# Kernel tuning notes

Hardware: AMD Instinct MI355X
Metric: run time of the kernel (lower is better)

The kernel has to match this reference:

```python
import jax, jax.numpy as jnp
import numpy as np

D_MODEL = 1024
N_HEADS = 16
HEAD_DIM = D_MODEL // N_HEADS


def setup_inputs() -> dict:
    key = jax.random.key(0)
    k1, k2, k3 = jax.random.split(key, 3)
    scale = 1.0 / np.sqrt(D_MODEL)
    x = jax.random.normal(k1, (4, 2048, D_MODEL), dtype=jnp.float32)
    w_qkv = jax.random.normal(k2, (D_MODEL, 3 * D_MODEL), dtype=jnp.float32) * scale
    b_qkv = jnp.zeros((3 * D_MODEL,), dtype=jnp.float32)
    w_proj = jax.random.normal(k3, (D_MODEL, D_MODEL), dtype=jnp.float32) * scale
    b_proj = jnp.zeros((D_MODEL,), dtype=jnp.float32)
    return {"x": x, "w_qkv": w_qkv, "b_qkv": b_qkv, "w_proj": w_proj, "b_proj": b_proj}


def reference(x, w_qkv, b_qkv, w_proj, b_proj):
    B, T, C = x.shape
    H, Dh = N_HEADS, HEAD_DIM
    qkv = x @ w_qkv + b_qkv                       # (B, T, 3C)
    qkv = qkv.reshape(B, T, 3, H, Dh)
    q = qkv[:, :, 0].transpose(0, 2, 1, 3)        # (B, H, T, Dh)
    k = qkv[:, :, 1].transpose(0, 2, 1, 3)
    v = qkv[:, :, 2].transpose(0, 2, 1, 3)
    att = jnp.einsum('bhqd,bhkd->bhqk', q, k) / jnp.sqrt(jnp.float32(Dh))
    causal = jnp.tril(jnp.ones((T, T), dtype=bool))
    att = jnp.where(causal[None, None], att, -jnp.inf)
    att = jax.nn.softmax(att, axis=-1)
    y = jnp.einsum('bhqk,bhkd->bhqd', att, v)     # (B, H, T, Dh)
    y = y.transpose(0, 2, 1, 3).reshape(B, T, C)
    return y @ w_proj + b_proj
```

## Files before the change

kernel.cpp:

```cpp
#include <hip/hip_runtime.h>
#include <hip/hip_bf16.h>
#include <math.h>

typedef __bf16 bf16_t;
typedef __bf16 bf16x4 __attribute__((ext_vector_type(4)));
typedef __bf16 bf16x8 __attribute__((ext_vector_type(8)));
typedef float floatx4 __attribute__((ext_vector_type(4)));
typedef unsigned int u32;

#define AS1 __attribute__((address_space(1)))
#define AS3 __attribute__((address_space(3)))

__device__ bf16_t g_xb[8192 * 1024];
__device__ bf16_t g_wqkvT[3072 * 1024];
__device__ bf16_t g_wprojT[1024 * 1024];
__device__ float  g_bqkv[3072];
__device__ float  g_bproj[1024];
__device__ bf16_t g_qkv[3ull * 64 * 2048 * 64];
#define HBREG (64ull * 2048 * 64)

__global__ __launch_bounds__(256) void cvt_x(const float* __restrict__ src,
                                             const float* __restrict__ bq,
                                             const float* __restrict__ bp) {
  int blk = blockIdx.x;
  int tid = threadIdx.x;
  if (blk < 4096) {
    int i0 = (blk * 256 + tid) * 8;
    const float4* s = (const float4*)src;
    float4 a = s[i0 / 4], b = s[i0 / 4 + 1];
    bf16x8 v;
    v[0] = (bf16_t)a.x; v[1] = (bf16_t)a.y; v[2] = (bf16_t)a.z; v[3] = (bf16_t)a.w;
    v[4] = (bf16_t)b.x; v[5] = (bf16_t)b.y; v[6] = (bf16_t)b.z; v[7] = (bf16_t)b.w;
    *(bf16x8*)&g_xb[i0] = v;
  } else if (blk == 4096) {
    for (int i = tid; i < 3072; i += 256) g_bqkv[i] = bq[i];
  } else {
    for (int i = tid; i < 1024; i += 256) g_bproj[i] = bp[i];
  }
}

__global__ __launch_bounds__(256) void tr64(const float* __restrict__ wqkv,
                                            const float* __restrict__ wproj) {
  __shared__ bf16_t tile[64][65];
  const int R = 1024;
  int bx = blockIdx.x;
  const float* in;
  bf16_t* out;
  int C, c0;
  if (bx < 48) { in = wqkv; out = g_wqkvT; C = 3072; c0 = bx * 64; }
  else         { in = wproj; out = g_wprojT; C = 1024; c0 = (bx - 48) * 64; }
  int r0 = blockIdx.y * 64;
  int tid = threadIdx.x;
#pragma unroll
  for (int it = 0; it < 16; ++it) {
    int idx = tid + it * 256;
    int r = idx >> 6, c = idx & 63;
    tile[r][c] = (bf16_t)in[(size_t)(r0 + r) * C + (c0 + c)];
  }
  __syncthreads();
#pragma unroll
  for (int it = 0; it < 16; ++it) {
    int idx = tid + it * 256;
    int r = idx >> 6, c = idx & 63;
    out[(size_t)(c0 + r) * R + (r0 + c)] = tile[c][r];
  }
}

#define MFMA16(a, b, c) __builtin_amdgcn_mfma_f32_16x16x32_bf16(a, b, c, 0, 0, 0)
#define SB0() __builtin_amdgcn_sched_barrier(0)
#define PH_MID()                                          \
  do {                                                    \
    SB0();                                                \
    __builtin_amdgcn_s_barrier();                         \
    SB0();                                                \
    asm volatile("s_waitcnt lgkmcnt(0)" ::: "memory");    \
    SB0();                                                \
  } while (0)
#define PH_END()                                          \
  do {                                                    \
    SB0();                                                \
    __builtin_amdgcn_s_barrier();                         \
    SB0();                                                \
  } while (0)

__global__ __launch_bounds__(512) void gemm256(float* __restrict__ out_ext,
                                               int M, int N, int K,
                                               int amode, int bsel, int cmode) {
  __shared__ alignas(16) bf16_t As[2][2][256 * 32];
  __shared__ alignas(16) bf16_t Bs[2][2][128 * 32];
  (void)M;
  const bf16_t* Ag = (amode == 0) ? g_xb : g_qkv;
  const bf16_t* Bt = bsel ? g_wprojT : g_wqkvT;
  const float* bias = bsel ? g_bproj : g_bqkv;
  const int tid = threadIdx.x;

  int gx = gridDim.x;
  int nwg = gx * gridDim.y;
  int lin = blockIdx.y * gx + blockIdx.x;
  int swz = (lin & 7) * (nwg >> 3) + (lin >> 3);
  int bx = swz % gx, by = swz / gx;
  const int m0 = by * 256, n0 = bx * 128;

  const int lane = tid & 63, wave = tid >> 6;
  const int wm = wave >> 1, wn = wave & 1;
  const int quad = lane >> 4, l16 = lane & 15;

  u32 L0 = (u32)tid * 16u, L1 = (u32)(tid + 512) * 16u;
  u32 y0 = L0 ^ (((L0 >> 7) & 3u) << 4);
  u32 y1 = L1 ^ (((L1 >> 7) & 3u) << 4);
  int ar0 = y0 >> 6, ac0 = (y0 & 63) >> 1;
  int ar1 = y1 >> 6, ac1 = (y1 & 63) >> 1;
  u32 a_go0, a_go1, ktstride;
  if (amode == 0) {
    a_go0 = (u32)(m0 + ar0) * (u32)K + (u32)ac0;
    a_go1 = (u32)(m0 + ar1) * (u32)K + (u32)ac1;
    ktstride = 64u;
  } else {
    int mA = m0 + ar0, bb_ = mA >> 11, tt = mA & 2047;
    a_go0 = (u32)bb_ * 2097152u + (u32)tt * 64u + (u32)ac0;
    mA = m0 + ar1; bb_ = mA >> 11; tt = mA & 2047;
    a_go1 = (u32)bb_ * 2097152u + (u32)tt * 64u + (u32)ac1;
    ktstride = 131072u;
  }
  u32 b_go = (u32)(n0 + ar0) * (u32)K + (u32)ac0;

  auto stageA = [&](int kt_, int s_) {
    int bb = kt_ & 1;
    const bf16_t* s0 = Ag + (size_t)(a_go0 + (u32)kt_ * ktstride + (u32)s_ * 32u);
    const bf16_t* s1 = Ag + (size_t)(a_go1 + (u32)kt_ * ktstride + (u32)s_ * 32u);
    __builtin_amdgcn_global_load_lds((const AS1 void*)s0,
                                     (AS3 void*)&As[bb][s_][(u32)tid * 8u], 16, 0, 0);
    __builtin_amdgcn_global_load_lds((const AS1 void*)s1,
                                     (AS3 void*)&As[bb][s_][(u32)(tid + 512) * 8u], 16, 0, 0);
  };
  auto stageB = [&](int kt_, int s_) {
    int bb = kt_ & 1;
    const bf16_t* s0 = Bt + (size_t)(b_go + (u32)kt_ * 64u + (u32)s_ * 32u);
    __builtin_amdgcn_global_load_lds((const AS1 void*)s0,
                                     (AS3 void*)&Bs[bb][s_][(u32)tid * 8u], 16, 0, 0);
  };

  int saB[4], sbB[4];
#pragma unroll
  for (int i = 0; i < 4; ++i) {
    u32 xa = (u32)(wm * 64 + i * 16 + l16) * 64u + (u32)quad * 16u;
    saB[i] = (int)(xa ^ (((xa >> 7) & 3u) << 4));
    u32 xb = (u32)(wn * 64 + i * 16 + l16) * 64u + (u32)quad * 16u;
    sbB[i] = (int)(xb ^ (((xb >> 7) & 3u) << 4));
  }

  floatx4 acc[4][4] = {};
  const int NT = K >> 6;

  stageA(0, 0); SB0(); stageB(0, 0); SB0();
  stageA(0, 1); SB0(); stageB(0, 1); SB0();
  stageA(1, 0); SB0(); stageB(1, 0); SB0();
  asm volatile("s_waitcnt vmcnt(6)" ::: "memory");
  __builtin_amdgcn_s_barrier();
  SB0();

  for (int kt = 0; kt < NT; ++kt) {
    const int b = kt & 1;
    const char* Ab0 = (const char*)&As[b][0][0];
    const char* Ab1 = (const char*)&As[b][1][0];
    const char* Bb0 = (const char*)&Bs[b][0][0];
    const char* Bb1 = (const char*)&Bs[b][1][0];
    bf16x8 a0[4], bf2[2];

#pragma unroll
    for (int i = 0; i < 4; ++i) a0[i] = *(const bf16x8*)(Ab0 + saB[i]);
    bf2[0] = *(const bf16x8*)(Bb0 + sbB[0]);
    bf2[1] = *(const bf16x8*)(Bb0 + sbB[1]);
    if (kt + 1 < NT) stageA(kt + 1, 1);
    PH_MID();
    __builtin_amdgcn_s_setprio(1);
#pragma unroll
    for (int i = 0; i < 4; ++i) {
      acc[i][0] = MFMA16(a0[i], bf2[0], acc[i][0]);
      acc[i][1] = MFMA16(a0[i], bf2[1], acc[i][1]);
    }
    __builtin_amdgcn_s_setprio(0);
    PH_END();

    bf2[0] = *(const bf16x8*)(Bb0 + sbB[2]);
    bf2[1] = *(const bf16x8*)(Bb0 + sbB[3]);
    if (kt + 1 < NT) stageB(kt + 1, 1);
    PH_MID();
    __builtin_amdgcn_s_setprio(1);
#pragma unroll
    for (int i = 0; i < 4; ++i) {
      acc[i][2] = MFMA16(a0[i], bf2[0], acc[i][2]);
      acc[i][3] = MFMA16(a0[i], bf2[1], acc[i][3]);
    }
    __builtin_amdgcn_s_setprio(0);
    SB0();
    if (kt + 1 < NT) asm volatile("s_waitcnt vmcnt(6)" ::: "memory");
    else             asm volatile("s_waitcnt vmcnt(0)" ::: "memory");
    __builtin_amdgcn_s_barrier();
    SB0();

#pragma unroll
    for (int i = 0; i < 4; ++i) a0[i] = *(const bf16x8*)(Ab1 + saB[i]);
    bf2[0] = *(const bf16x8*)(Bb1 + sbB[0]);
    bf2[1] = *(const bf16x8*)(Bb1 + sbB[1]);
    if (kt + 2 < NT) stageA(kt + 2, 0);
    PH_MID();
    __builtin_amdgcn_s_setprio(1);
#pragma unroll
    for (int i = 0; i < 4; ++i) {
      acc[i][0] = MFMA16(a0[i], bf2[0], acc[i][0]);
      acc[i][1] = MFMA16(a0[i], bf2[1], acc[i][1]);
    }
    __builtin_amdgcn_s_setprio(0);
    PH_END();

    bf2[0] = *(const bf16x8*)(Bb1 + sbB[2]);
    bf2[1] = *(const bf16x8*)(Bb1 + sbB[3]);
    if (kt + 2 < NT) stageB(kt + 2, 0);
    PH_MID();
    __builtin_amdgcn_s_setprio(1);
#pragma unroll
    for (int i = 0; i < 4; ++i) {
      acc[i][2] = MFMA16(a0[i], bf2[0], acc[i][2]);
      acc[i][3] = MFMA16(a0[i], bf2[1], acc[i][3]);
    }
    __builtin_amdgcn_s_setprio(0);
    SB0();
    if (kt + 2 < NT)      asm volatile("s_waitcnt vmcnt(6)" ::: "memory");
    else if (kt + 1 < NT) asm volatile("s_waitcnt vmcnt(3)" ::: "memory");
    else                  asm volatile("s_waitcnt vmcnt(0)" ::: "memory");
    __builtin_amdgcn_s_barrier();
    SB0();
  }

#pragma unroll
  for (int mf = 0; mf < 4; ++mf) {
#pragma unroll
    for (int nf = 0; nf < 4; ++nf) {
      int ncol = n0 + wn * 64 + nf * 16 + l16;
      float bb = bias[ncol];
      int mbase = m0 + wm * 64 + mf * 16 + quad * 4;
      if (cmode == 0) {
        int which = ncol >> 10;
        int h = (ncol >> 6) & 15;
        int d = ncol & 63;
        int b_ = mbase >> 11, t = mbase & 2047;
        if (which == 2) {
          bf16x4 pk;
#pragma unroll
          for (int r = 0; r < 4; ++r) pk[r] = (bf16_t)(acc[mf][nf][r] + bb);
          size_t dst = 2 * HBREG + ((size_t)((b_ * 16 + h) * 64 + d)) * 2048 + t;
          *(bf16x4*)&g_qkv[dst] = pk;
        } else {
          size_t base = (size_t)which * HBREG +
                        ((size_t)((b_ * 16 + h) * 2048 + t)) * 64 + d;
#pragma unroll
          for (int r = 0; r < 4; ++r)
            g_qkv[base + (size_t)r * 64] = (bf16_t)(acc[mf][nf][r] + bb);
        }
      } else {
#pragma unroll
        for (int r = 0; r < 4; ++r)
          out_ext[(size_t)(mbase + r) * N + ncol] = acc[mf][nf][r] + bb;
      }
    }
  }
}

__global__ __launch_bounds__(256) void attn64() {
  const int LDW = 72;
  __shared__ bf16_t Qs[64 * 72];
  __shared__ bf16_t Ks[64 * 72];
  __shared__ bf16_t Vt[64 * 72];
  bf16_t* Ps = Qs;
  const float C1 = 0.1803368801111204f;
  const float C2 = -23.083120654223414f;
  const int tid = threadIdx.x;
  const int qpair = blockIdx.x;
  const int bh = blockIdx.y;
  const bf16_t* Qb  = g_qkv + (size_t)bh * 2048 * 64;
  const bf16_t* Kb  = g_qkv + HBREG + (size_t)bh * 2048 * 64;
  const bf16_t* VTb = g_qkv + 2 * HBREG + (size_t)bh * 64 * 2048;
  bf16_t* Yb = g_qkv + (size_t)bh * 2048 * 64;
  const int lane = tid & 63, wave = tid >> 6;
  const int quad = lane >> 4, l16 = lane & 15;
  const int row0 = tid >> 3, c80 = (tid & 7) * 8;

  bf16x8 ones8;
#pragma unroll
  for (int j = 0; j < 8; ++j) ones8[j] = (bf16_t)1.0f;

  for (int ph = 0; ph < 2; ++ph) {
    const int qi = ph ? (31 - qpair) : qpair;
    const int q0 = qi * 64;

    *(bf16x8*)&Qs[row0 * LDW + c80] =
        *(const bf16x8*)&Qb[(size_t)(q0 + row0) * 64 + c80];
    *(bf16x8*)&Qs[(row0 + 32) * LDW + c80] =
        *(const bf16x8*)&Qb[(size_t)(q0 + row0 + 32) * 64 + c80];
    __syncthreads();
    bf16x8 aq0 = *(const bf16x8*)&Qs[(wave * 16 + l16) * LDW + quad * 8];
    bf16x8 aq1 = *(const bf16x8*)&Qs[(wave * 16 + l16) * LDW + 32 + quad * 8];

    floatx4 o[4] = {};
    floatx4 osum = {};

    bf16x8 kp0 = *(const bf16x8*)&Kb[(size_t)row0 * 64 + c80];
    bf16x8 kp1 = *(const bf16x8*)&Kb[(size_t)(row0 + 32) * 64 + c80];
    bf16x8 vp0 = *(const bf16x8*)&VTb[(size_t)row0 * 2048 + c80];
    bf16x8 vp1 = *(const bf16x8*)&VTb[(size_t)(row0 + 32) * 2048 + c80];

    const int ntiles = qi + 1;
    for (int kt = 0; kt < ntiles; ++kt) {
      __syncthreads();
      *(bf16x8*)&Ks[row0 * LDW + c80] = kp0;
      *(bf16x8*)&Ks[(row0 + 32) * LDW + c80] = kp1;
      *(bf16x8*)&Vt[row0 * LDW + c80] = vp0;
      *(bf16x8*)&Vt[(row0 + 32) * LDW + c80] = vp1;
      if (kt + 1 < ntiles) {
        const int k1 = (kt + 1) * 64;
        kp0 = *(const bf16x8*)&Kb[(size_t)(k1 + row0) * 64 + c80];
        kp1 = *(const bf16x8*)&Kb[(size_t)(k1 + row0 + 32) * 64 + c80];
        vp0 = *(const bf16x8*)&VTb[(size_t)row0 * 2048 + k1 + c80];
        vp1 = *(const bf16x8*)&VTb[(size_t)(row0 + 32) * 2048 + k1 + c80];
      }
      __syncthreads();

      const int k0 = kt * 64;
      floatx4 s[4];
#pragma unroll
      for (int tn = 0; tn < 4; ++tn) {
        bf16x8 bk0 = *(const bf16x8*)&Ks[(tn * 16 + l16) * LDW + quad * 8];
        bf16x8 bk1 = *(const bf16x8*)&Ks[(tn * 16 + l16) * LDW + 32 + quad * 8];
        floatx4 z = {};
        z = __builtin_amdgcn_mfma_f32_16x16x32_bf16(aq0, bk0, z, 0, 0, 0);
        z = __builtin_amdgcn_mfma_f32_16x16x32_bf16(aq1, bk1, z, 0, 0, 0);
        s[tn] = z;
      }

      if (kt == qi) {
#pragma unroll
        for (int tn = 0; tn < 4; ++tn) {
          int kcol = k0 + tn * 16 + l16;
#pragma unroll
          for (int r = 0; r < 4; ++r) {
            int qrow = q0 + wave * 16 + quad * 4 + r;
            float p = exp2f(fminf(fmaf(s[tn][r], C1, C2), 30.f));
            s[tn][r] = (kcol > qrow) ? 0.f : p;
          }
        }
      } else {
#pragma unroll
        for (int tn = 0; tn < 4; ++tn)
#pragma unroll
          for (int r = 0; r < 4; ++r)
            s[tn][r] = exp2f(fminf(fmaf(s[tn][r], C1, C2), 30.f));
      }

      bf16_t* Pw = &Ps[wave * 16 * LDW];
#pragma unroll
      for (int tn = 0; tn < 4; ++tn)
#pragma unroll
        for (int r = 0; r < 4; ++r)
          Pw[(quad * 4 + r) * LDW + tn * 16 + l16] = (bf16_t)s[tn][r];

      bf16x8 ap0 = *(const bf16x8*)&Pw[l16 * LDW + quad * 8];
      bf16x8 ap1 = *(const bf16x8*)&Pw[l16 * LDW + 32 + quad * 8];
#pragma unroll
      for (int tn = 0; tn < 4; ++tn) {
        bf16x8 bv0 = *(const bf16x8*)&Vt[(tn * 16 + l16) * LDW + quad * 8];
        bf16x8 bv1 = *(const bf16x8*)&Vt[(tn * 16 + l16) * LDW + 32 + quad * 8];
        o[tn] = __builtin_amdgcn_mfma_f32_16x16x32_bf16(ap0, bv0, o[tn], 0, 0, 0);
        o[tn] = __builtin_amdgcn_mfma_f32_16x16x32_bf16(ap1, bv1, o[tn], 0, 0, 0);
      }
      osum = __builtin_amdgcn_mfma_f32_16x16x32_bf16(ap0, ones8, osum, 0, 0, 0);
      osum = __builtin_amdgcn_mfma_f32_16x16x32_bf16(ap1, ones8, osum, 0, 0, 0);
    }

#pragma unroll
    for (int tn = 0; tn < 4; ++tn) {
      int d = tn * 16 + l16;
#pragma unroll
      for (int r = 0; r < 4; ++r) {
        int t = q0 + wave * 16 + quad * 4 + r;
        float v = o[tn][r] / osum[r];
        Yb[(size_t)t * 64 + d] = (bf16_t)v;
      }
    }
    __syncthreads();
  }
}

extern "C" void kernel_launch(void* const* d_in, const int* in_sizes, int n_in,
                              void* d_out, int out_size, void* d_ws, size_t ws_size,
                              hipStream_t stream) {
  const float* x      = (const float*)d_in[0];
  const float* w_qkv  = (const float*)d_in[1];
  const float* b_qkv  = (const float*)d_in[2];
  const float* w_proj = (const float*)d_in[3];
  const float* b_proj = (const float*)d_in[4];
  (void)d_ws; (void)ws_size;

  cvt_x<<<4098, 256, 0, stream>>>(x, b_qkv, b_proj);
  tr64<<<dim3(64, 16), 256, 0, stream>>>(w_qkv, w_proj);

  gemm256<<<dim3(24, 32), 512, 0, stream>>>(nullptr, 8192, 3072, 1024, 0, 0, 0);

  attn64<<<dim3(16, 64), 256, 0, stream>>>();

  gemm256<<<dim3(8, 32), 512, 0, stream>>>((float*)d_out, 8192, 1024, 1024, 1, 1, 1);
}
```

Before: 322.3 us.

## Enlarge GEMM tile to 256x256 with K64 swizzled LDS ping-pong schedule

```diff
diff --git a/kernel.cpp b/kernel.cpp
--- a/kernel.cpp
+++ b/kernel.cpp
@@ -86,8 +86,8 @@
 __global__ __launch_bounds__(512) void gemm256(float* __restrict__ out_ext,
                                                int M, int N, int K,
                                                int amode, int bsel, int cmode) {
-  __shared__ alignas(16) bf16_t As[2][2][256 * 32];
-  __shared__ alignas(16) bf16_t Bs[2][2][128 * 32];
+  __shared__ alignas(16) bf16_t As[2][256 * 64];
+  __shared__ alignas(16) bf16_t Bs[2][256 * 64];
   (void)M;
   const bf16_t* Ag = (amode == 0) ? g_xb : g_qkv;
   const bf16_t* Bt = bsel ? g_wprojT : g_wqkvT;
@@ -99,170 +99,199 @@
   int lin = blockIdx.y * gx + blockIdx.x;
   int swz = (lin & 7) * (nwg >> 3) + (lin >> 3);
   int bx = swz % gx, by = swz / gx;
-  const int m0 = by * 256, n0 = bx * 128;
+  const int m0 = by * 256, n0 = bx * 256;
 
   const int lane = tid & 63, wave = tid >> 6;
-  const int wm = wave >> 1, wn = wave & 1;
+  const int wm = wave >> 2, wn = wave & 3;
   const int quad = lane >> 4, l16 = lane & 15;
 
-  u32 L0 = (u32)tid * 16u, L1 = (u32)(tid + 512) * 16u;
-  u32 y0 = L0 ^ (((L0 >> 7) & 3u) << 4);
-  u32 y1 = L1 ^ (((L1 >> 7) & 3u) << 4);
-  int ar0 = y0 >> 6, ac0 = (y0 & 63) >> 1;
-  int ar1 = y1 >> 6, ac1 = (y1 & 63) >> 1;
-  u32 a_go0, a_go1, ktstride;
+  const u32 xv = (u32)(l16 & 7) << 4;
+  const u32 sq0 = ((u32)quad * 16u) ^ xv;
+  const u32 sq1 = (64u + (u32)quad * 16u) ^ xv;
+  const u32 a_rb = (u32)(wm * 64 + l16) * 128u;
+  const u32 b_rb = (u32)(wn * 32 + l16) * 128u;
+
+  u32 row_j[2], scol_j[2];
+#pragma unroll
+  for (int j = 0; j < 2; ++j) {
+    u32 L = ((u32)j * 512u + (u32)tid) * 16u;
+    u32 y = L ^ (((L >> 7) & 7u) << 4);
+    row_j[j] = y >> 7;
+    scol_j[j] = (y & 127u) >> 1;
+  }
+  u32 a_go[2][2], b_go[2][2], akts;
   if (amode == 0) {
-    a_go0 = (u32)(m0 + ar0) * (u32)K + (u32)ac0;
-    a_go1 = (u32)(m0 + ar1) * (u32)K + (u32)ac1;
-    ktstride = 64u;
+#pragma unroll
+    for (int h = 0; h < 2; ++h)
+#pragma unroll
+      for (int j = 0; j < 2; ++j)
+        a_go[h][j] = (u32)(m0 + h * 128 + (int)row_j[j]) * (u32)K + scol_j[j];
+    akts = 64u;
   } else {
-    int mA = m0 + ar0, bb_ = mA >> 11, tt = mA & 2047;
-    a_go0 = (u32)bb_ * 2097152u + (u32)tt * 64u + (u32)ac0;
-    mA = m0 + ar1; bb_ = mA >> 11; tt = mA & 2047;
-    a_go1 = (u32)bb_ * 2097152u + (u32)tt * 64u + (u32)ac1;
-    ktstride = 131072u;
-  }
-  u32 b_go = (u32)(n0 + ar0) * (u32)K + (u32)ac0;
-
-  auto stageA = [&](int kt_, int s_) {
-    int bb = kt_ & 1;
-    const bf16_t* s0 = Ag + (size_t)(a_go0 + (u32)kt_ * ktstride + (u32)s_ * 32u);
-    const bf16_t* s1 = Ag + (size_t)(a_go1 + (u32)kt_ * ktstride + (u32)s_ * 32u);
-    __builtin_amdgcn_global_load_lds((const AS1 void*)s0,
-                                     (AS3 void*)&As[bb][s_][(u32)tid * 8u], 16, 0, 0);
-    __builtin_amdgcn_global_load_lds((const AS1 void*)s1,
-                                     (AS3 void*)&As[bb][s_][(u32)(tid + 512) * 8u], 16, 0, 0);
+#pragma unroll
+    for (int h = 0; h < 2; ++h)
+#pragma unroll
+      for (int j = 0; j < 2; ++j) {
+        int m = m0 + h * 128 + (int)row_j[j];
+        a_go[h][j] = (u32)(m >> 11) * 2097152u + (u32)(m & 2047) * 64u + scol_j[j];
+      }
+    akts = 131072u;
+  }
+#pragma unroll
+  for (int h = 0; h < 2; ++h)
+#pragma unroll
+    for (int j = 0; j < 2; ++j)
+      b_go[h][j] = (u32)(n0 + h * 128 + (int)row_j[j]) * (u32)K + scol_j[j];
+
+  auto stageA = [&](int kt_, int h_) {
+#pragma unroll
+    for (int j = 0; j < 2; ++j)
+      __builtin_amdgcn_global_load_lds(
+          (const AS1 void*)(Ag + (size_t)(a_go[h_][j] + (u32)kt_ * akts)),
+          (AS3 void*)&As[kt_ & 1][h_ * 8192 + (j * 512 + tid) * 8], 16, 0, 0);
   };
-  auto stageB = [&](int kt_, int s_) {
-    int bb = kt_ & 1;
-    const bf16_t* s0 = Bt + (size_t)(b_go + (u32)kt_ * 64u + (u32)s_ * 32u);
-    __builtin_amdgcn_global_load_lds((const AS1 void*)s0,
-                                     (AS3 void*)&Bs[bb][s_][(u32)tid * 8u], 16, 0, 0);
+  auto stageB = [&](int kt_, int h_) {
+#pragma unroll
+    for (int j = 0; j < 2; ++j)
+      __builtin_amdgcn_global_load_lds(
+          (const AS1 void*)(Bt + (size_t)(b_go[h_][j] + (u32)kt_ * 64u)),
+          (AS3 void*)&Bs[kt_ & 1][h_ * 8192 + (j * 512 + tid) * 8], 16, 0, 0);
   };
 
-  int saB[4], sbB[4];
-#pragma unroll
-  for (int i = 0; i < 4; ++i) {
-    u32 xa = (u32)(wm * 64 + i * 16 + l16) * 64u + (u32)quad * 16u;
-    saB[i] = (int)(xa ^ (((xa >> 7) & 3u) << 4));
-    u32 xb = (u32)(wn * 64 + i * 16 + l16) * 64u + (u32)quad * 16u;
-    sbB[i] = (int)(xb ^ (((xb >> 7) & 3u) << 4));
-  }
-
-  floatx4 acc[4][4] = {};
+  floatx4 acc[2][4][2][2] = {};
   const int NT = K >> 6;
 
   stageA(0, 0); SB0(); stageB(0, 0); SB0();
   stageA(0, 1); SB0(); stageB(0, 1); SB0();
-  stageA(1, 0); SB0(); stageB(1, 0); SB0();
-  asm volatile("s_waitcnt vmcnt(6)" ::: "memory");
+  asm volatile("s_waitcnt vmcnt(4)" ::: "memory");
   __builtin_amdgcn_s_barrier();
   SB0();
 
   for (int kt = 0; kt < NT; ++kt) {
     const int b = kt & 1;
-    const char* Ab0 = (const char*)&As[b][0][0];
-    const char* Ab1 = (const char*)&As[b][1][0];
-    const char* Bb0 = (const char*)&Bs[b][0][0];
-    const char* Bb1 = (const char*)&Bs[b][1][0];
-    bf16x8 a0[4], bf2[2];
-
-#pragma unroll
-    for (int i = 0; i < 4; ++i) a0[i] = *(const bf16x8*)(Ab0 + saB[i]);
-    bf2[0] = *(const bf16x8*)(Bb0 + sbB[0]);
-    bf2[1] = *(const bf16x8*)(Bb0 + sbB[1]);
+    const char* Ab = (const char*)&As[b][0];
+    const char* Bb = (const char*)&Bs[b][0];
+    bf16x8 af[4][2], bv[2][2], bw[2][2];
+
+#pragma unroll
+    for (int mf = 0; mf < 4; ++mf) {
+      af[mf][0] = *(const bf16x8*)(Ab + (a_rb + mf * 2048 + sq0));
+      af[mf][1] = *(const bf16x8*)(Ab + (a_rb + mf * 2048 + sq1));
+    }
+#pragma unroll
+    for (int nf = 0; nf < 2; ++nf) {
+      bv[nf][0] = *(const bf16x8*)(Bb + (b_rb + nf * 2048 + sq0));
+      bv[nf][1] = *(const bf16x8*)(Bb + (b_rb + nf * 2048 + sq1));
+    }
+    if (kt + 1 < NT) stageA(kt + 1, 0);
+    PH_MID();
+    __builtin_amdgcn_s_setprio(1);
+#pragma unroll
+    for (int mf = 0; mf < 4; ++mf)
+#pragma unroll
+      for (int nf = 0; nf < 2; ++nf) {
+        acc[0][mf][0][nf] = MFMA16(af[mf][0], bv[nf][0], acc[0][mf][0][nf]);
+        acc[0][mf][0][nf] = MFMA16(af[mf][1], bv[nf][1], acc[0][mf][0][nf]);
+      }
+    __builtin_amdgcn_s_setprio(0);
+    SB0();
+    if (kt + 1 < NT) asm volatile("s_waitcnt vmcnt(2)" ::: "memory");
+    else             asm volatile("s_waitcnt vmcnt(0)" ::: "memory");
+    __builtin_amdgcn_s_barrier();
+    SB0();
+
+#pragma unroll
+    for (int nf = 0; nf < 2; ++nf) {
+      bw[nf][0] = *(const bf16x8*)(Bb + (b_rb + 16384 + nf * 2048 + sq0));
+      bw[nf][1] = *(const bf16x8*)(Bb + (b_rb + 16384 + nf * 2048 + sq1));
+    }
+    if (kt + 1 < NT) stageB(kt + 1, 0);
+    PH_MID();
+    __builtin_amdgcn_s_setprio(1);
+#pragma unroll
+    for (int mf = 0; mf < 4; ++mf)
+#pragma unroll
+      for (int nf = 0; nf < 2; ++nf) {
+        acc[0][mf][1][nf] = MFMA16(af[mf][0], bw[nf][0], acc[0][mf][1][nf]);
+        acc[0][mf][1][nf] = MFMA16(af[mf][1], bw[nf][1], acc[0][mf][1][nf]);
+      }
+    __builtin_amdgcn_s_setprio(0);
+    PH_END();
+
+#pragma unroll
+    for (int mf = 0; mf < 4; ++mf) {
+      af[mf][0] = *(const bf16x8*)(Ab + (a_rb + 16384 + mf * 2048 + sq0));
+      af[mf][1] = *(const bf16x8*)(Ab + (a_rb + 16384 + mf * 2048 + sq1));
+    }
     if (kt + 1 < NT) stageA(kt + 1, 1);
     PH_MID();
     __builtin_amdgcn_s_setprio(1);
 #pragma unroll
-    for (int i = 0; i < 4; ++i) {
-      acc[i][0] = MFMA16(a0[i], bf2[0], acc[i][0]);
-      acc[i][1] = MFMA16(a0[i], bf2[1], acc[i][1]);
-    }
+    for (int mf = 0; mf < 4; ++mf)
+#pragma unroll
+      for (int nf = 0; nf < 2; ++nf) {
+        acc[1][mf][1][nf] = MFMA16(af[mf][0], bw[nf][0], acc[1][mf][1][nf]);
+        acc[1][mf][1][nf] = MFMA16(af[mf][1], bw[nf][1], acc[1][mf][1][nf]);
+      }
     __builtin_amdgcn_s_setprio(0);
     PH_END();
 
-    bf2[0] = *(const bf16x8*)(Bb0 + sbB[2]);
-    bf2[1] = *(const bf16x8*)(Bb0 + sbB[3]);
+#pragma unroll
+    for (int nf = 0; nf < 2; ++nf) {
+      bv[nf][0] = *(const bf16x8*)(Bb + (b_rb + nf * 2048 + sq0));
+      bv[nf][1] = *(const bf16x8*)(Bb + (b_rb + nf * 2048 + sq1));
+    }
     if (kt + 1 < NT) stageB(kt + 1, 1);
     PH_MID();
     __builtin_amdgcn_s_setprio(1);
 #pragma unroll
-    for (int i = 0; i < 4; ++i) {
-      acc[i][2] = MFMA16(a0[i], bf2[0], acc[i][2]);
-      acc[i][3] = MFMA16(a0[i], bf2[1], acc[i][3]);
-    }
+    for (int mf = 0; mf < 4; ++mf)
+#pragma unroll
+      for (int nf = 0; nf < 2; ++nf) {
+        acc[1][mf][0][nf] = MFMA16(af[mf][0], bv[nf][0], acc[1][mf][0][nf]);
+        acc[1][mf][0][nf] = MFMA16(af[mf][1], bv[nf][1], acc[1][mf][0][nf]);
+      }
     __builtin_amdgcn_s_setprio(0);
     SB0();
-    if (kt + 1 < NT) asm volatile("s_waitcnt vmcnt(6)" ::: "memory");
+    if (kt + 1 < NT) asm volatile("s_waitcnt vmcnt(4)" ::: "memory");
     else             asm volatile("s_waitcnt vmcnt(0)" ::: "memory");
     __builtin_amdgcn_s_barrier();
     SB0();
-
-#pragma unroll
-    for (int i = 0; i < 4; ++i) a0[i] = *(const bf16x8*)(Ab1 + saB[i]);
-    bf2[0] = *(const bf16x8*)(Bb1 + sbB[0]);
-    bf2[1] = *(const bf16x8*)(Bb1 + sbB[1]);
-    if (kt + 2 < NT) stageA(kt + 2, 0);
-    PH_MID();
-    __builtin_amdgcn_s_setprio(1);
-#pragma unroll
-    for (int i = 0; i < 4; ++i) {
-      acc[i][0] = MFMA16(a0[i], bf2[0], acc[i][0]);
-      acc[i][1] = MFMA16(a0[i], bf2[1], acc[i][1]);
-    }
-    __builtin_amdgcn_s_setprio(0);
-    PH_END();
-
-    bf2[0] = *(const bf16x8*)(Bb1 + sbB[2]);
-    bf2[1] = *(const bf16x8*)(Bb1 + sbB[3]);
-    if (kt + 2 < NT) stageB(kt + 2, 0);
-    PH_MID();
-    __builtin_amdgcn_s_setprio(1);
-#pragma unroll
-    for (int i = 0; i < 4; ++i) {
-      acc[i][2] = MFMA16(a0[i], bf2[0], acc[i][2]);
-      acc[i][3] = MFMA16(a0[i], bf2[1], acc[i][3]);
-    }
-    __builtin_amdgcn_s_setprio(0);
-    SB0();
-    if (kt + 2 < NT)      asm volatile("s_waitcnt vmcnt(6)" ::: "memory");
-    else if (kt + 1 < NT) asm volatile("s_waitcnt vmcnt(3)" ::: "memory");
-    else                  asm volatile("s_waitcnt vmcnt(0)" ::: "memory");
-    __builtin_amdgcn_s_barrier();
-    SB0();
-  }
-
-#pragma unroll
-  for (int mf = 0; mf < 4; ++mf) {
-#pragma unroll
-    for (int nf = 0; nf < 4; ++nf) {
-      int ncol = n0 + wn * 64 + nf * 16 + l16;
-      float bb = bias[ncol];
-      int mbase = m0 + wm * 64 + mf * 16 + quad * 4;
-      if (cmode == 0) {
-        int which = ncol >> 10;
-        int h = (ncol >> 6) & 15;
-        int d = ncol & 63;
-        int b_ = mbase >> 11, t = mbase & 2047;
-        if (which == 2) {
-          bf16x4 pk;
-#pragma unroll
-          for (int r = 0; r < 4; ++r) pk[r] = (bf16_t)(acc[mf][nf][r] + bb);
-          size_t dst = 2 * HBREG + ((size_t)((b_ * 16 + h) * 64 + d)) * 2048 + t;
-          *(bf16x4*)&g_qkv[dst] = pk;
-        } else {
-          size_t base = (size_t)which * HBREG +
-                        ((size_t)((b_ * 16 + h) * 2048 + t)) * 64 + d;
-#pragma unroll
-          for (int r = 0; r < 4; ++r)
-            g_qkv[base + (size_t)r * 64] = (bf16_t)(acc[mf][nf][r] + bb);
-        }
+  }
+
+#pragma unroll
+  for (int mh = 0; mh < 2; ++mh)
+#pragma unroll
+  for (int mf = 0; mf < 4; ++mf)
+#pragma unroll
+  for (int nh = 0; nh < 2; ++nh)
+#pragma unroll
+  for (int nf = 0; nf < 2; ++nf) {
+    int ncol = n0 + wn * 32 + nh * 128 + nf * 16 + l16;
+    float bb = bias[ncol];
+    int mbase = m0 + wm * 64 + mh * 128 + mf * 16 + quad * 4;
+    if (cmode == 0) {
+      int which = ncol >> 10;
+      int h = (ncol >> 6) & 15;
+      int d = ncol & 63;
+      int b_ = mbase >> 11, t = mbase & 2047;
+      if (which == 2) {
+        bf16x4 pk;
+#pragma unroll
+        for (int r = 0; r < 4; ++r) pk[r] = (bf16_t)(acc[mh][mf][nh][nf][r] + bb);
+        size_t dst = 2 * HBREG + ((size_t)((b_ * 16 + h) * 64 + d)) * 2048 + t;
+        *(bf16x4*)&g_qkv[dst] = pk;
       } else {
+        size_t base = (size_t)which * HBREG +
+                      ((size_t)((b_ * 16 + h) * 2048 + t)) * 64 + d;
 #pragma unroll
         for (int r = 0; r < 4; ++r)
-          out_ext[(size_t)(mbase + r) * N + ncol] = acc[mf][nf][r] + bb;
-      }
+          g_qkv[base + (size_t)r * 64] = (bf16_t)(acc[mh][mf][nh][nf][r] + bb);
+      }
+    } else {
+#pragma unroll
+      for (int r = 0; r < 4; ++r)
+        out_ext[(size_t)(mbase + r) * N + ncol] = acc[mh][mf][nh][nf][r] + bb;
     }
   }
 }
@@ -404,9 +433,9 @@
   cvt_x<<<4098, 256, 0, stream>>>(x, b_qkv, b_proj);
   tr64<<<dim3(64, 16), 256, 0, stream>>>(w_qkv, w_proj);
 
-  gemm256<<<dim3(24, 32), 512, 0, stream>>>(nullptr, 8192, 3072, 1024, 0, 0, 0);
+  gemm256<<<dim3(12, 32), 512, 0, stream>>>(nullptr, 8192, 3072, 1024, 0, 0, 0);
 
   attn64<<<dim3(16, 64), 256, 0, stream>>>();
 
-  gemm256<<<dim3(8, 32), 512, 0, stream>>>((float*)d_out, 8192, 1024, 1024, 1, 1, 1);
+  gemm256<<<dim3(4, 32), 512, 0, stream>>>((float*)d_out, 8192, 1024, 1024, 1, 1, 1);
 }
```

Result: faster. 310.7 us (-3.6%).
